# Optimization experiments

Measured on AMD Instinct MI355X. Metric: run time of the kernel, lower is better.

The kernel has to match this reference:

```python
import jax, jax.numpy as jnp
import numpy as np

B, S, D, H = 2, 2048, 1024, 16
HD = D // H  # head_dim = 64
ROPE_BASE = 10000.0


def _rope_cos_sin(seq_len, head_dim, dtype):
    inv_freq = 1.0 / (ROPE_BASE ** (jnp.arange(0, head_dim, 2, dtype=jnp.float32) / head_dim))
    t = jnp.arange(seq_len, dtype=jnp.float32)
    freqs = jnp.einsum('i,j->ij', t, inv_freq)            # [S, HD/2]
    emb = jnp.concatenate([freqs, freqs], axis=-1)        # [S, HD]
    return jnp.cos(emb).astype(dtype), jnp.sin(emb).astype(dtype)


def _rotate_half(x):
    x1, x2 = jnp.split(x, 2, axis=-1)
    return jnp.concatenate([-x2, x1], axis=-1)


def setup_inputs() -> dict:
    key = jax.random.key(0)
    ks = jax.random.split(key, 5)
    scale = 1.0 / np.sqrt(D)
    x = jax.random.normal(ks[0], (B, S, D), dtype=jnp.float32)
    wq = jax.random.normal(ks[1], (D, D), dtype=jnp.float32) * scale
    wk = jax.random.normal(ks[2], (D, D), dtype=jnp.float32) * scale
    wv = jax.random.normal(ks[3], (D, D), dtype=jnp.float32) * scale
    wo = jax.random.normal(ks[4], (D, D), dtype=jnp.float32) * scale
    # causal additive mask: 0 on/below diagonal, -1e9 above
    causal = jnp.triu(jnp.full((S, S), -1e9, dtype=jnp.float32), k=1)
    attention_mask = causal[None, None, :, :]
    return {'x': x, 'attention_mask': attention_mask, 'wq': wq, 'wk': wk, 'wv': wv, 'wo': wo}


def reference(x, attention_mask, wq, wk, wv, wo):
    b, s, d = x.shape
    scale = 1.0 / np.sqrt(HD)
    # projections (torch Linear: y = x @ W.T)
    q = (x @ wq.T).reshape(b, s, H, HD).transpose(0, 2, 1, 3)  # [B,H,S,HD]
    k = (x @ wk.T).reshape(b, s, H, HD).transpose(0, 2, 1, 3)
    v = (x @ wv.T).reshape(b, s, H, HD).transpose(0, 2, 1, 3)
    cos, sin = _rope_cos_sin(s, HD, x.dtype)                   # [S, HD]
    cos = cos[None, None]
    sin = sin[None, None]
    q = q * cos + _rotate_half(q) * sin
    k = k * cos + _rotate_half(k) * sin
    scores = jnp.einsum('bhqd,bhkd->bhqk', q, k) * scale       # [B,H,S,S]
    scores = scores + attention_mask
    probs = jax.nn.softmax(scores, axis=-1)
    out = jnp.einsum('bhqk,bhkd->bhqd', probs, v)              # [B,H,S,HD]
    out = out.transpose(0, 2, 1, 3).reshape(b, s, d)
    return out @ wo.T
```

## Files before the change

### kernel.cpp

```cpp
#include <hip/hip_runtime.h>
#include <cstdint>
#include <cstddef>

typedef __attribute__((ext_vector_type(8))) _Float16 half8;
typedef __attribute__((ext_vector_type(4))) _Float16 half4;
typedef __attribute__((ext_vector_type(2))) __fp16 fp16x2;
typedef __attribute__((ext_vector_type(4))) float f32x4;

#define NB 2
#define NS 2048
#define ND 1024
#define NH 16
#define NHD 64
#define NM (NB * NS)

__device__ __forceinline__ void cvt8(const float* __restrict__ s,
                                     _Float16* __restrict__ d, int g) {
  const float4* s4 = (const float4*)s + (size_t)g * 2;
  float4 a = s4[0], b = s4[1];
  half8 h;
  h[0] = (_Float16)a.x; h[1] = (_Float16)a.y;
  h[2] = (_Float16)a.z; h[3] = (_Float16)a.w;
  h[4] = (_Float16)b.x; h[5] = (_Float16)b.y;
  h[6] = (_Float16)b.z; h[7] = (_Float16)b.w;
  *(half8*)(d + (size_t)g * 8) = h;
}

__global__ void prep(const float* __restrict__ x,
                     const float* __restrict__ wq, const float* __restrict__ wk,
                     const float* __restrict__ wv, const float* __restrict__ wo,
                     _Float16* __restrict__ xb,
                     _Float16* __restrict__ wqb, _Float16* __restrict__ wkb,
                     _Float16* __restrict__ wvb, _Float16* __restrict__ wob,
                     float* __restrict__ cosT, float* __restrict__ sinT) {
  int i = blockIdx.x * 256 + threadIdx.x;
  if (i < 524288) {
    cvt8(x, xb, i);
  } else if (i < 1048576) {
    int j = i - 524288;
    int k = j >> 17, g = j & 131071;
    const float* ws = (k == 0) ? wq : (k == 1) ? wk : (k == 2) ? wv : wo;
    _Float16* wd = (k == 0) ? wqb : (k == 1) ? wkb : (k == 2) ? wvb : wob;
    cvt8(ws, wd, g);
  } else if (i < 1056768) {
    int t0 = (i - 1048576) * 8;
#pragma unroll
    for (int e = 0; e < 8; ++e) {
      int t = t0 + e;
      int s = t >> 5, j = t & 31;
      float inv = expf(-(float)(2 * j) * (9.210340371976184f / 64.0f));
      float ang = (float)s * inv;
      cosT[t] = cosf(ang);
      sinT[t] = sinf(ang);
    }
  }
}

__device__ __forceinline__ void gload_lds16(const void* g, void* lds) {
  __builtin_amdgcn_global_load_lds(
      (const __attribute__((address_space(1))) unsigned int*)g,
      (__attribute__((address_space(3))) unsigned int*)lds, 16, 0, 0);
}

__device__ __forceinline__ float exp2_fast(float x) {
  float r;
  asm("v_exp_f32 %0, %1" : "=v"(r) : "v"(x));
  return r;
}

__device__ __forceinline__ void gemm_mainloop64(const _Float16* __restrict__ A,
                                                const _Float16* __restrict__ Bw,
                                                _Float16* As, _Float16* Bs,
                                                int brow, int bcol,
                                                int lane, int wid, int tid,
                                                f32x4 acc[4][4]) {
  const int l15 = lane & 15, l4 = lane >> 4;
  const int wr = wid >> 1, wc = wid & 1;
  const int rswz = (l15 & 7) << 4;
  const int srb = tid >> 3;
  const int scb = (tid & 7) * 16;

  for (int kt = 0; kt < ND / 64; ++kt) {
    const int k0 = kt * 64;
#pragma unroll
    for (int c = 0; c < 4; ++c) {
      const int r = c * 32 + srb;
      const int sb = scb ^ ((r & 7) << 4);
      gload_lds16((const char*)(A + (size_t)(brow + r) * ND + k0) + sb,
                  (char*)As + c * 4096 + tid * 16);
      gload_lds16((const char*)(Bw + (size_t)(bcol + r) * ND + k0) + sb,
                  (char*)Bs + c * 4096 + tid * 16);
    }
    __syncthreads();
#pragma unroll
    for (int kk = 0; kk < 2; ++kk) {
      half8 af[4], bf[4];
#pragma unroll
      for (int m = 0; m < 4; ++m) {
        const int row = wr * 64 + m * 16 + l15;
        af[m] = *(const half8*)((const char*)As +
                 ((row * 128 + kk * 64 + l4 * 16) ^ rswz));
      }
#pragma unroll
      for (int n = 0; n < 4; ++n) {
        const int row = wc * 64 + n * 16 + l15;
        bf[n] = *(const half8*)((const char*)Bs +
                 ((row * 128 + kk * 64 + l4 * 16) ^ rswz));
      }
#pragma unroll
      for (int m = 0; m < 4; ++m)
#pragma unroll
        for (int n = 0; n < 4; ++n)
          acc[m][n] = __builtin_amdgcn_mfma_f32_16x16x32_f16(af[m], bf[n],
                                                             acc[m][n], 0, 0, 0);
    }
    __syncthreads();
  }
}

__launch_bounds__(256, 3)
__global__ void qkv_gemm(const _Float16* __restrict__ X,
                         const _Float16* __restrict__ Wq,
                         const _Float16* __restrict__ Wk,
                         const _Float16* __restrict__ Wv,
                         _Float16* __restrict__ Qb,
                         _Float16* __restrict__ Kb,
                         _Float16* __restrict__ Vt,
                         const float* __restrict__ cosT,
                         const float* __restrict__ sinT) {
  __shared__ __align__(16) _Float16 As[128 * 64];
  __shared__ __align__(16) _Float16 Bs[128 * 64];
  const int tid = threadIdx.x, lane = tid & 63, wid = tid >> 6;
  const int l15 = lane & 15, l4 = lane >> 4;
  const int wr = wid >> 1, wc = wid & 1;
  const int brow = blockIdx.y * 128, bcol = blockIdx.x * 128;
  const int mode = blockIdx.z;
  const _Float16* W = (mode == 0) ? Wq : (mode == 1 ? Wk : Wv);

  f32x4 acc[4][4] = {};
  gemm_mainloop64(X, W, As, Bs, brow, bcol, lane, wid, tid, acc);

  const int b = brow >> 11;
  const int sbase = (brow & (NS - 1)) + wr * 64;
  const int h = (bcol >> 6) + wc;

  if (mode < 2) {
    _Float16* oh = ((mode == 0) ? Qb : Kb) + (size_t)(b * NH + h) * NS * NHD;
#pragma unroll
    for (int m = 0; m < 4; ++m) {
#pragma unroll
      for (int r = 0; r < 4; ++r) {
        const int s = sbase + m * 16 + l4 * 4 + r;
#pragma unroll
        for (int n = 0; n < 2; ++n) {
          const int hd = n * 16 + l15;
          const float c = cosT[s * 32 + hd];
          const float sn = sinT[s * 32 + hd];
          const float lo = acc[m][n][r], hi = acc[m][n + 2][r];
          oh[(size_t)s * NHD + hd]      = (_Float16)(lo * c - hi * sn);
          oh[(size_t)s * NHD + hd + 32] = (_Float16)(hi * c + lo * sn);
        }
      }
    }
  } else {
#pragma unroll
    for (int m = 0; m < 4; ++m) {
      const int s0 = sbase + m * 16 + l4 * 4;
      const int npos = (s0 & ~63) + (m >> 1) * 32 + l4 * 8 + (m & 1) * 4;
#pragma unroll
      for (int n = 0; n < 4; ++n) {
        const int hd = n * 16 + l15;
        half4 pk;
        pk[0] = (_Float16)acc[m][n][0];
        pk[1] = (_Float16)acc[m][n][1];
        pk[2] = (_Float16)acc[m][n][2];
        pk[3] = (_Float16)acc[m][n][3];
        *(half4*)(Vt + ((size_t)(b * NH + h) * NHD + hd) * NS + npos) = pk;
      }
    }
  }
}

__launch_bounds__(256, 5)
__global__ void flash_attn(const _Float16* __restrict__ Qb,
                           const _Float16* __restrict__ Kb,
                           const _Float16* __restrict__ Vt,
                           _Float16* __restrict__ Ob) {
  __shared__ __align__(16) _Float16 Ks[2][64 * 64];
  __shared__ __align__(16) _Float16 Vs[2][64 * 64];
  const int tid = threadIdx.x, lane = tid & 63, wid = tid >> 6;
  const int l15 = lane & 15, l4 = lane >> 4;
  const int bh = blockIdx.x & 31;
  const int qt = 31 - (blockIdx.x >> 5);
  const _Float16* Qh = Qb + (size_t)bh * NS * NHD;
  const char* Kg = (const char*)(Kb + (size_t)bh * NS * NHD);
  const char* Vg = (const char*)(Vt + (size_t)bh * NHD * NS);

  const float K1 = 0.125f * 1.4426950408889634f;
  const int swz_lane = ((lane >> 3) & 7) << 4;
  const int qloc = wid * 16 + l15;
  const int rswz = (l15 & 7) << 4;
  const int b = bh >> 4, h = bh & 15;
  const int nkt = qt + 1;

  half8 qf[2];
#pragma unroll
  for (int kk = 0; kk < 2; ++kk)
    qf[kk] = *(const half8*)&Qh[(size_t)(qt * 64 + wid * 16 + l15) * NHD + kk * 32 + l4 * 8];

  f32x4 oacc[4] = {};
  float mrun = -3.0e38f, lrun = 0.f;

#pragma unroll
  for (int c = 0; c < 2; ++c) {
    const int chunk = wid * 2 + c;
    const int slot = chunk * 1024 + lane * 16;
    const int sw = slot ^ swz_lane;
    gload_lds16(Kg + sw, (char*)&Ks[0][0] + slot);
    const int vrow = slot >> 7;
    gload_lds16(Vg + (size_t)vrow * (NS * 2) + (sw & 127), (char*)&Vs[0][0] + slot);
  }
  __syncthreads();

  int cur = 0;
  for (int kt = 0; kt < nkt; ++kt) {
    if (kt + 1 < nkt) {
      const size_t knext = (size_t)(kt + 1);
#pragma unroll
      for (int c = 0; c < 2; ++c) {
        const int chunk = wid * 2 + c;
        const int slot = chunk * 1024 + lane * 16;
        const int sw = slot ^ swz_lane;
        gload_lds16(Kg + knext * 8192 + sw, (char*)&Ks[cur ^ 1][0] + slot);
        const int vrow = slot >> 7;
        gload_lds16(Vg + (size_t)vrow * (NS * 2) + knext * 128 + (sw & 127),
                    (char*)&Vs[cur ^ 1][0] + slot);
      }
    }

    const bool diag = (kt == qt);
    const char* Kbuf = (const char*)&Ks[cur][0];
    const char* Vbuf = (const char*)&Vs[cur][0];

    f32x4 sacc[4] = {};
    __builtin_amdgcn_s_setprio(1);
#pragma unroll
    for (int kk = 0; kk < 2; ++kk) {
#pragma unroll
      for (int n = 0; n < 4; ++n) {
        if (diag && n > wid) continue;
        const int off = ((n * 16 + l15) * 128 + kk * 64 + l4 * 16) ^ rswz;
        half8 kf = *(const half8*)(Kbuf + off);
        sacc[n] = __builtin_amdgcn_mfma_f32_16x16x32_f16(kf, qf[kk], sacc[n], 0, 0, 0);
      }
    }
    __builtin_amdgcn_s_setprio(0);

    float traw[16];
#pragma unroll
    for (int n = 0; n < 4; ++n)
#pragma unroll
      for (int r = 0; r < 4; ++r) {
        float v = sacc[n][r];
        if (diag) {
          const int ki = n * 16 + l4 * 4 + r;
          v = (ki > qloc) ? -3.0e38f : v;
        }
        traw[n * 4 + r] = v;
      }
    float mx = traw[0];
#pragma unroll
    for (int j = 1; j < 16; ++j) mx = fmaxf(mx, traw[j]);
    mx = fmaxf(mx, __shfl_xor(mx, 16, 64));
    mx = fmaxf(mx, __shfl_xor(mx, 32, 64));
    mx *= K1;
    const float mnew = fmaxf(mrun, mx);
    const float alpha = exp2_fast(mrun - mnew);
    mrun = mnew;
    float ps[16], rs = 0.f;
#pragma unroll
    for (int j = 0; j < 16; ++j) {
      ps[j] = exp2_fast(__builtin_fmaf(traw[j], K1, -mnew));
      rs += ps[j];
    }
    rs += __shfl_xor(rs, 16, 64);
    rs += __shfl_xor(rs, 32, 64);
    lrun = lrun * alpha + rs;
#pragma unroll
    for (int n = 0; n < 4; ++n) oacc[n] *= alpha;

    __builtin_amdgcn_s_setprio(1);
#pragma unroll
    for (int c = 0; c < 2; ++c) {
      if (diag && c == 1 && wid < 2) continue;
      half8 pb;
#pragma unroll
      for (int q2 = 0; q2 < 4; ++q2) {
        fp16x2 pp = __builtin_amdgcn_cvt_pkrtz(ps[8 * c + 2 * q2],
                                               ps[8 * c + 2 * q2 + 1]);
        pb[2 * q2]     = (_Float16)pp[0];
        pb[2 * q2 + 1] = (_Float16)pp[1];
      }
#pragma unroll
      for (int n = 0; n < 4; ++n) {
        const int off = ((n * 16 + l15) * 128 + c * 64 + l4 * 16) ^ rswz;
        half8 va = *(const half8*)(Vbuf + off);
        oacc[n] = __builtin_amdgcn_mfma_f32_16x16x32_f16(va, pb, oacc[n], 0, 0, 0);
      }
    }
    __builtin_amdgcn_s_setprio(0);

    __syncthreads();
    cur ^= 1;
  }

  const int s = qt * 64 + wid * 16 + l15;
  const float invl = 1.0f / lrun;
#pragma unroll
  for (int n = 0; n < 4; ++n) {
    f32x4 ov = oacc[n] * invl;
    half4 o;
    o[0] = (_Float16)ov[0];
    o[1] = (_Float16)ov[1];
    o[2] = (_Float16)ov[2];
    o[3] = (_Float16)ov[3];
    *(half4*)&Ob[((size_t)(b * NS + s)) * ND + h * NHD + n * 16 + l4 * 4] = o;
  }
}

__launch_bounds__(256, 2)
__global__ void proj_gemm(const _Float16* __restrict__ A,
                          const _Float16* __restrict__ W,
                          float* __restrict__ out) {
  __shared__ __align__(16) _Float16 As[128 * 64];
  __shared__ __align__(16) _Float16 Bs[64 * 64];
  const int tid = threadIdx.x, lane = tid & 63, wid = tid >> 6;
  const int l15 = lane & 15, l4 = lane >> 4;
  const int wr = wid >> 1, wc = wid & 1;
  const int brow = blockIdx.y * 128, bcol = blockIdx.x * 64;
  const int rswz = (l15 & 7) << 4;
  const int srb = tid >> 3;
  const int scb = (tid & 7) * 16;

  f32x4 acc[4][2] = {};
  for (int kt = 0; kt < ND / 64; ++kt) {
    const int k0 = kt * 64;
#pragma unroll
    for (int c = 0; c < 4; ++c) {
      const int r = c * 32 + srb;
      const int sb = scb ^ ((r & 7) << 4);
      gload_lds16((const char*)(A + (size_t)(brow + r) * ND + k0) + sb,
                  (char*)As + c * 4096 + tid * 16);
    }
#pragma unroll
    for (int c = 0; c < 2; ++c) {
      const int r = c * 32 + srb;
      const int sb = scb ^ ((r & 7) << 4);
      gload_lds16((const char*)(W + (size_t)(bcol + r) * ND + k0) + sb,
                  (char*)Bs + c * 4096 + tid * 16);
    }
    __syncthreads();
#pragma unroll
    for (int kk = 0; kk < 2; ++kk) {
      half8 af[4], bf[2];
#pragma unroll
      for (int m = 0; m < 4; ++m) {
        const int row = wr * 64 + m * 16 + l15;
        af[m] = *(const half8*)((const char*)As +
                 ((row * 128 + kk * 64 + l4 * 16) ^ rswz));
      }
#pragma unroll
      for (int n = 0; n < 2; ++n) {
        const int row = wc * 32 + n * 16 + l15;
        bf[n] = *(const half8*)((const char*)Bs +
                 ((row * 128 + kk * 64 + l4 * 16) ^ rswz));
      }
#pragma unroll
      for (int m = 0; m < 4; ++m)
#pragma unroll
        for (int n = 0; n < 2; ++n)
          acc[m][n] = __builtin_amdgcn_mfma_f32_16x16x32_f16(af[m], bf[n],
                                                             acc[m][n], 0, 0, 0);
    }
    __syncthreads();
  }
#pragma unroll
  for (int m = 0; m < 4; ++m)
#pragma unroll
    for (int n = 0; n < 2; ++n)
#pragma unroll
      for (int r = 0; r < 4; ++r)
        out[(size_t)(brow + wr * 64 + m * 16 + l4 * 4 + r) * ND
            + bcol + wc * 32 + n * 16 + l15] = acc[m][n][r];
}

extern "C" void kernel_launch(void* const* d_in, const int* in_sizes, int n_in,
                              void* d_out, int out_size, void* d_ws, size_t ws_size,
                              hipStream_t stream) {
  const float* x  = (const float*)d_in[0];
  const float* wq = (const float*)d_in[2];
  const float* wk = (const float*)d_in[3];
  const float* wv = (const float*)d_in[4];
  const float* wo = (const float*)d_in[5];
  float* out = (float*)d_out;

  char* w = (char*)d_ws;
  _Float16* xb   = (_Float16*)(w);
  _Float16* wqb  = (_Float16*)(w + (8ull  << 20));
  _Float16* wkb  = (_Float16*)(w + (10ull << 20));
  _Float16* wvb  = (_Float16*)(w + (12ull << 20));
  _Float16* wob  = (_Float16*)(w + (14ull << 20));
  _Float16* Qb   = (_Float16*)(w + (16ull << 20));
  _Float16* Kb   = (_Float16*)(w + (24ull << 20));
  _Float16* Vt   = (_Float16*)(w + (32ull << 20));
  _Float16* Ob   = (_Float16*)(w + (40ull << 20));
  float*    cosT = (float*)   (w + (48ull << 20));
  float*    sinT = (float*)   (w + (48ull << 20) + (1ull << 18));

  dim3 blk(256);
  prep<<<4128, blk, 0, stream>>>(x, wq, wk, wv, wo, xb, wqb, wkb, wvb, wob,
                                 cosT, sinT);
  qkv_gemm<<<dim3(8, 32, 3), blk, 0, stream>>>(xb, wqb, wkb, wvb, Qb, Kb, Vt,
                                               cosT, sinT);
  flash_attn<<<1024, blk, 0, stream>>>(Qb, Kb, Vt, Ob);
  proj_gemm<<<dim3(16, 32), blk, 0, stream>>>(Ob, wob, out);
}
```

Baseline: 99.62 us.

## Double key tile to 128 in flash attention with templated masked last tile

The flash attention loop now processes 128-key tiles instead of 64, halving the number of iterations, barriers and online-softmax rescales per query tile. The tile body moves into a template so only the final tile pays for causal masking and for skipping work above the diagonal. The V staging layout and swizzle are reworked for the wider tile. LDS use doubles and the launch-bounds occupancy hint drops from 5 to 2 blocks, which adds register pressure and reduces latency hiding.

```diff
diff --git a/kernel.cpp b/kernel.cpp
--- a/kernel.cpp
+++ b/kernel.cpp
@@ -181,13 +181,89 @@
   }
 }
 
-__launch_bounds__(256, 5)
+template <bool MASKED>
+__device__ __forceinline__ void attn_tile(const char* Kbuf, const char* Vbuf,
+                                          const half8* qf, f32x4* oacc,
+                                          float& mrun, float& lrun,
+                                          int kbase, int qmaxw, int qglob,
+                                          int l15, int l4, int rswz, float K1) {
+  f32x4 sacc[8] = {};
+  __builtin_amdgcn_s_setprio(1);
+#pragma unroll
+  for (int kk = 0; kk < 2; ++kk) {
+#pragma unroll
+    for (int n = 0; n < 8; ++n) {
+      if (MASKED && kbase + n * 16 > qmaxw) continue;
+      const int off = ((n * 16 + l15) * 128 + kk * 64 + l4 * 16) ^ rswz;
+      half8 kf = *(const half8*)(Kbuf + off);
+      sacc[n] = __builtin_amdgcn_mfma_f32_16x16x32_f16(kf, qf[kk], sacc[n], 0, 0, 0);
+    }
+  }
+  __builtin_amdgcn_s_setprio(0);
+
+  float traw[32];
+#pragma unroll
+  for (int n = 0; n < 8; ++n)
+#pragma unroll
+    for (int r = 0; r < 4; ++r) {
+      float v = sacc[n][r];
+      if (MASKED) {
+        const int kg = kbase + n * 16 + l4 * 4 + r;
+        v = (kg > qglob) ? -3.0e38f : v;
+      }
+      traw[n * 4 + r] = v;
+    }
+  float mx = traw[0];
+#pragma unroll
+  for (int j = 1; j < 32; ++j) mx = fmaxf(mx, traw[j]);
+  mx = fmaxf(mx, __shfl_xor(mx, 16, 64));
+  mx = fmaxf(mx, __shfl_xor(mx, 32, 64));
+  mx *= K1;
+  const float mnew = fmaxf(mrun, mx);
+  const float alpha = exp2_fast(mrun - mnew);
+  mrun = mnew;
+  float ps[32], rs = 0.f;
+#pragma unroll
+  for (int j = 0; j < 32; ++j) {
+    ps[j] = exp2_fast(__builtin_fmaf(traw[j], K1, -mnew));
+    rs += ps[j];
+  }
+  rs += __shfl_xor(rs, 16, 64);
+  rs += __shfl_xor(rs, 32, 64);
+  lrun = lrun * alpha + rs;
+#pragma unroll
+  for (int n = 0; n < 4; ++n) oacc[n] *= alpha;
+
+  __builtin_amdgcn_s_setprio(1);
+#pragma unroll
+  for (int c = 0; c < 4; ++c) {
+    if (MASKED && kbase + c * 32 > qmaxw) continue;
+    half8 pb;
+#pragma unroll
+    for (int q2 = 0; q2 < 4; ++q2) {
+      fp16x2 pp = __builtin_amdgcn_cvt_pkrtz(ps[8 * c + 2 * q2],
+                                             ps[8 * c + 2 * q2 + 1]);
+      pb[2 * q2]     = (_Float16)pp[0];
+      pb[2 * q2 + 1] = (_Float16)pp[1];
+    }
+#pragma unroll
+    for (int n = 0; n < 4; ++n) {
+      const int off = (n * 16 + l15) * 256 + (c >> 1) * 128
+                    + (((c & 1) * 64 + l4 * 16) ^ rswz);
+      half8 va = *(const half8*)(Vbuf + off);
+      oacc[n] = __builtin_amdgcn_mfma_f32_16x16x32_f16(va, pb, oacc[n], 0, 0, 0);
+    }
+  }
+  __builtin_amdgcn_s_setprio(0);
+}
+
+__launch_bounds__(256, 2)
 __global__ void flash_attn(const _Float16* __restrict__ Qb,
                            const _Float16* __restrict__ Kb,
                            const _Float16* __restrict__ Vt,
                            _Float16* __restrict__ Ob) {
-  __shared__ __align__(16) _Float16 Ks[2][64 * 64];
-  __shared__ __align__(16) _Float16 Vs[2][64 * 64];
+  __shared__ __align__(16) _Float16 Ks[2][128 * 64];
+  __shared__ __align__(16) _Float16 Vs[2][64 * 128];
   const int tid = threadIdx.x, lane = tid & 63, wid = tid >> 6;
   const int l15 = lane & 15, l4 = lane >> 4;
   const int bh = blockIdx.x & 31;
@@ -198,123 +274,50 @@
 
   const float K1 = 0.125f * 1.4426950408889634f;
   const int swz_lane = ((lane >> 3) & 7) << 4;
-  const int qloc = wid * 16 + l15;
   const int rswz = (l15 & 7) << 4;
   const int b = bh >> 4, h = bh & 15;
-  const int nkt = qt + 1;
+  const int nt = (qt >> 1) + 1;
+  const int kbase_last = (nt - 1) * 128;
+  const int qglob = qt * 64 + wid * 16 + l15;
+  const int qmaxw = qt * 64 + wid * 16 + 15;
 
   half8 qf[2];
 #pragma unroll
   for (int kk = 0; kk < 2; ++kk)
-    qf[kk] = *(const half8*)&Qh[(size_t)(qt * 64 + wid * 16 + l15) * NHD + kk * 32 + l4 * 8];
+    qf[kk] = *(const half8*)&Qh[(size_t)qglob * NHD + kk * 32 + l4 * 8];
 
   f32x4 oacc[4] = {};
   float mrun = -3.0e38f, lrun = 0.f;
 
-#pragma unroll
-  for (int c = 0; c < 2; ++c) {
-    const int chunk = wid * 2 + c;
-    const int slot = chunk * 1024 + lane * 16;
-    const int sw = slot ^ swz_lane;
-    gload_lds16(Kg + sw, (char*)&Ks[0][0] + slot);
-    const int vrow = slot >> 7;
-    gload_lds16(Vg + (size_t)vrow * (NS * 2) + (sw & 127), (char*)&Vs[0][0] + slot);
-  }
+  auto stage = [&](int t, int si) {
+#pragma unroll
+    for (int c = 0; c < 4; ++c) {
+      const int chunk = wid * 4 + c;
+      const int slot = chunk * 1024 + lane * 16;
+      const int sw = slot ^ swz_lane;
+      gload_lds16(Kg + (size_t)t * 16384 + sw, (char*)&Ks[si][0] + slot);
+      const int vrow = slot >> 8;
+      const int vhalf = (slot >> 7) & 1;
+      const int vinner = slot & 127;
+      gload_lds16(Vg + (size_t)vrow * (NS * 2) + t * 256 + vhalf * 128
+                     + (vinner ^ ((vrow & 7) << 4)),
+                  (char*)&Vs[si][0] + slot);
+    }
+  };
+
+  stage(0, 0);
   __syncthreads();
-
   int cur = 0;
-  for (int kt = 0; kt < nkt; ++kt) {
-    if (kt + 1 < nkt) {
-      const size_t knext = (size_t)(kt + 1);
-#pragma unroll
-      for (int c = 0; c < 2; ++c) {
-        const int chunk = wid * 2 + c;
-        const int slot = chunk * 1024 + lane * 16;
-        const int sw = slot ^ swz_lane;
-        gload_lds16(Kg + knext * 8192 + sw, (char*)&Ks[cur ^ 1][0] + slot);
-        const int vrow = slot >> 7;
-        gload_lds16(Vg + (size_t)vrow * (NS * 2) + knext * 128 + (sw & 127),
-                    (char*)&Vs[cur ^ 1][0] + slot);
-      }
-    }
-
-    const bool diag = (kt == qt);
-    const char* Kbuf = (const char*)&Ks[cur][0];
-    const char* Vbuf = (const char*)&Vs[cur][0];
-
-    f32x4 sacc[4] = {};
-    __builtin_amdgcn_s_setprio(1);
-#pragma unroll
-    for (int kk = 0; kk < 2; ++kk) {
-#pragma unroll
-      for (int n = 0; n < 4; ++n) {
-        if (diag && n > wid) continue;
-        const int off = ((n * 16 + l15) * 128 + kk * 64 + l4 * 16) ^ rswz;
-        half8 kf = *(const half8*)(Kbuf + off);
-        sacc[n] = __builtin_amdgcn_mfma_f32_16x16x32_f16(kf, qf[kk], sacc[n], 0, 0, 0);
-      }
-    }
-    __builtin_amdgcn_s_setprio(0);
-
-    float traw[16];
-#pragma unroll
-    for (int n = 0; n < 4; ++n)
-#pragma unroll
-      for (int r = 0; r < 4; ++r) {
-        float v = sacc[n][r];
-        if (diag) {
-          const int ki = n * 16 + l4 * 4 + r;
-          v = (ki > qloc) ? -3.0e38f : v;
-        }
-        traw[n * 4 + r] = v;
-      }
-    float mx = traw[0];
-#pragma unroll
-    for (int j = 1; j < 16; ++j) mx = fmaxf(mx, traw[j]);
-    mx = fmaxf(mx, __shfl_xor(mx, 16, 64));
-    mx = fmaxf(mx, __shfl_xor(mx, 32, 64));
-    mx *= K1;
-    const float mnew = fmaxf(mrun, mx);
-    const float alpha = exp2_fast(mrun - mnew);
-    mrun = mnew;
-    float ps[16], rs = 0.f;
-#pragma unroll
-    for (int j = 0; j < 16; ++j) {
-      ps[j] = exp2_fast(__builtin_fmaf(traw[j], K1, -mnew));
-      rs += ps[j];
-    }
-    rs += __shfl_xor(rs, 16, 64);
-    rs += __shfl_xor(rs, 32, 64);
-    lrun = lrun * alpha + rs;
-#pragma unroll
-    for (int n = 0; n < 4; ++n) oacc[n] *= alpha;
-
-    __builtin_amdgcn_s_setprio(1);
-#pragma unroll
-    for (int c = 0; c < 2; ++c) {
-      if (diag && c == 1 && wid < 2) continue;
-      half8 pb;
-#pragma unroll
-      for (int q2 = 0; q2 < 4; ++q2) {
-        fp16x2 pp = __builtin_amdgcn_cvt_pkrtz(ps[8 * c + 2 * q2],
-                                               ps[8 * c + 2 * q2 + 1]);
-        pb[2 * q2]     = (_Float16)pp[0];
-        pb[2 * q2 + 1] = (_Float16)pp[1];
-      }
-#pragma unroll
-      for (int n = 0; n < 4; ++n) {
-        const int off = ((n * 16 + l15) * 128 + c * 64 + l4 * 16) ^ rswz;
-        half8 va = *(const half8*)(Vbuf + off);
-        oacc[n] = __builtin_amdgcn_mfma_f32_16x16x32_f16(va, pb, oacc[n], 0, 0, 0);
-      }
-    }
-    __builtin_amdgcn_s_setprio(0);
-
+  for (int t = 0; t + 1 < nt; ++t) {
+    stage(t + 1, cur ^ 1);
+    attn_tile<false>((const char*)&Ks[cur][0], (const char*)&Vs[cur][0], qf,
+                     oacc, mrun, lrun, 0, 0, 0, l15, l4, rswz, K1);
     __syncthreads();
     cur ^= 1;
   }
-
-  const int s = qt * 64 + wid * 16 + l15;
+  attn_tile<true>((const char*)&Ks[cur][0], (const char*)&Vs[cur][0], qf,
+                  oacc, mrun, lrun, kbase_last, qmaxw, qglob, l15, l4, rswz, K1);
+
   const float invl = 1.0f / lrun;
 #pragma unroll
   for (int n = 0; n < 4; ++n) {
@@ -324,7 +327,7 @@
     o[1] = (_Float16)ov[1];
     o[2] = (_Float16)ov[2];
     o[3] = (_Float16)ov[3];
-    *(half4*)&Ob[((size_t)(b * NS + s)) * ND + h * NHD + n * 16 + l4 * 4] = o;
+    *(half4*)&Ob[((size_t)(b * NS + qglob)) * ND + h * NHD + n * 16 + l4 * 4] = o;
   }
 }
 
```

Measured after the change: 122.3 us. 22.8% more time.

## Share K/V tile loads across two query tiles per 512-thread flash block

Applied to the files above, without the earlier changes.

Each flash-attention block now has 8 waves and covers 128 query rows (two 64-row sub-tiles), so every staged K/V tile in LDS serves both sub-tiles and global K/V traffic per query drops by about half. The grid shrinks to 512 blocks, and each wave loads one chunk per stage instead of two. The first sub-tile's waves sit idle through the final key tile, where only the second sub-tile still has work, while still joining the barriers. Fewer, larger blocks can also leave the causal work less evenly balanced across CUs.

```diff
diff --git a/kernel.cpp b/kernel.cpp
--- a/kernel.cpp
+++ b/kernel.cpp
@@ -181,7 +181,7 @@
   }
 }
 
-__launch_bounds__(256, 5)
+__launch_bounds__(512, 6)
 __global__ void flash_attn(const _Float16* __restrict__ Qb,
                            const _Float16* __restrict__ Kb,
                            const _Float16* __restrict__ Vt,
@@ -190,131 +190,124 @@
   __shared__ __align__(16) _Float16 Vs[2][64 * 64];
   const int tid = threadIdx.x, lane = tid & 63, wid = tid >> 6;
   const int l15 = lane & 15, l4 = lane >> 4;
+  const int sub = wid >> 2, w4 = wid & 3;
   const int bh = blockIdx.x & 31;
-  const int qt = 31 - (blockIdx.x >> 5);
+  const int qt2 = 15 - (blockIdx.x >> 5);
   const _Float16* Qh = Qb + (size_t)bh * NS * NHD;
   const char* Kg = (const char*)(Kb + (size_t)bh * NS * NHD);
   const char* Vg = (const char*)(Vt + (size_t)bh * NHD * NS);
 
   const float K1 = 0.125f * 1.4426950408889634f;
   const int swz_lane = ((lane >> 3) & 7) << 4;
-  const int qloc = wid * 16 + l15;
+  const int qloc = w4 * 16 + l15;
   const int rswz = (l15 & 7) << 4;
   const int b = bh >> 4, h = bh & 15;
-  const int nkt = qt + 1;
+  const int nkt = 2 * qt2 + 2;
+  const int mylim = 2 * qt2 + sub;
+  const int qglob = qt2 * 128 + sub * 64 + w4 * 16 + l15;
 
   half8 qf[2];
 #pragma unroll
   for (int kk = 0; kk < 2; ++kk)
-    qf[kk] = *(const half8*)&Qh[(size_t)(qt * 64 + wid * 16 + l15) * NHD + kk * 32 + l4 * 8];
+    qf[kk] = *(const half8*)&Qh[(size_t)qglob * NHD + kk * 32 + l4 * 8];
 
   f32x4 oacc[4] = {};
   float mrun = -3.0e38f, lrun = 0.f;
 
-#pragma unroll
-  for (int c = 0; c < 2; ++c) {
-    const int chunk = wid * 2 + c;
-    const int slot = chunk * 1024 + lane * 16;
+  auto stage = [&](int t, int si) {
+    const int slot = wid * 1024 + lane * 16;
     const int sw = slot ^ swz_lane;
-    gload_lds16(Kg + sw, (char*)&Ks[0][0] + slot);
+    gload_lds16(Kg + (size_t)t * 8192 + sw, (char*)&Ks[si][0] + slot);
     const int vrow = slot >> 7;
-    gload_lds16(Vg + (size_t)vrow * (NS * 2) + (sw & 127), (char*)&Vs[0][0] + slot);
-  }
+    gload_lds16(Vg + (size_t)vrow * (NS * 2) + t * 128 + (sw & 127),
+                (char*)&Vs[si][0] + slot);
+  };
+
+  stage(0, 0);
   __syncthreads();
 
   int cur = 0;
   for (int kt = 0; kt < nkt; ++kt) {
-    if (kt + 1 < nkt) {
-      const size_t knext = (size_t)(kt + 1);
+    if (kt + 1 < nkt) stage(kt + 1, cur ^ 1);
+
+    if (kt <= mylim) {
+      const bool diag = (kt == mylim);
+      const char* Kbuf = (const char*)&Ks[cur][0];
+      const char* Vbuf = (const char*)&Vs[cur][0];
+
+      f32x4 sacc[4] = {};
+      __builtin_amdgcn_s_setprio(1);
+#pragma unroll
+      for (int kk = 0; kk < 2; ++kk) {
+#pragma unroll
+        for (int n = 0; n < 4; ++n) {
+          if (diag && n > w4) continue;
+          const int off = ((n * 16 + l15) * 128 + kk * 64 + l4 * 16) ^ rswz;
+          half8 kf = *(const half8*)(Kbuf + off);
+          sacc[n] = __builtin_amdgcn_mfma_f32_16x16x32_f16(kf, qf[kk], sacc[n], 0, 0, 0);
+        }
+      }
+      __builtin_amdgcn_s_setprio(0);
+
+      float traw[16];
+#pragma unroll
+      for (int n = 0; n < 4; ++n)
+#pragma unroll
+        for (int r = 0; r < 4; ++r) {
+          float v = sacc[n][r];
+          if (diag) {
+            const int ki = n * 16 + l4 * 4 + r;
+            v = (ki > qloc) ? -3.0e38f : v;
+          }
+          traw[n * 4 + r] = v;
+        }
+      float mx = traw[0];
+#pragma unroll
+      for (int j = 1; j < 16; ++j) mx = fmaxf(mx, traw[j]);
+      mx = fmaxf(mx, __shfl_xor(mx, 16, 64));
+      mx = fmaxf(mx, __shfl_xor(mx, 32, 64));
+      mx *= K1;
+      const float mnew = fmaxf(mrun, mx);
+      const float alpha = exp2_fast(mrun - mnew);
+      mrun = mnew;
+      float ps[16], rs = 0.f;
+#pragma unroll
+      for (int j = 0; j < 16; ++j) {
+        ps[j] = exp2_fast(__builtin_fmaf(traw[j], K1, -mnew));
+        rs += ps[j];
+      }
+      rs += __shfl_xor(rs, 16, 64);
+      rs += __shfl_xor(rs, 32, 64);
+      lrun = lrun * alpha + rs;
+#pragma unroll
+      for (int n = 0; n < 4; ++n) oacc[n] *= alpha;
+
+      __builtin_amdgcn_s_setprio(1);
 #pragma unroll
       for (int c = 0; c < 2; ++c) {
-        const int chunk = wid * 2 + c;
-        const int slot = chunk * 1024 + lane * 16;
-        const int sw = slot ^ swz_lane;
-        gload_lds16(Kg + knext * 8192 + sw, (char*)&Ks[cur ^ 1][0] + slot);
-        const int vrow = slot >> 7;
-        gload_lds16(Vg + (size_t)vrow * (NS * 2) + knext * 128 + (sw & 127),
-                    (char*)&Vs[cur ^ 1][0] + slot);
-      }
-    }
-
-    const bool diag = (kt == qt);
-    const char* Kbuf = (const char*)&Ks[cur][0];
-    const char* Vbuf = (const char*)&Vs[cur][0];
-
-    f32x4 sacc[4] = {};
-    __builtin_amdgcn_s_setprio(1);
-#pragma unroll
-    for (int kk = 0; kk < 2; ++kk) {
-#pragma unroll
-      for (int n = 0; n < 4; ++n) {
-        if (diag && n > wid) continue;
-        const int off = ((n * 16 + l15) * 128 + kk * 64 + l4 * 16) ^ rswz;
-        half8 kf = *(const half8*)(Kbuf + off);
-        sacc[n] = __builtin_amdgcn_mfma_f32_16x16x32_f16(kf, qf[kk], sacc[n], 0, 0, 0);
-      }
-    }
-    __builtin_amdgcn_s_setprio(0);
-
-    float traw[16];
-#pragma unroll
-    for (int n = 0; n < 4; ++n)
-#pragma unroll
-      for (int r = 0; r < 4; ++r) {
-        float v = sacc[n][r];
-        if (diag) {
-          const int ki = n * 16 + l4 * 4 + r;
-          v = (ki > qloc) ? -3.0e38f : v;
+        if (diag && c == 1 && w4 < 2) continue;
+        half8 pb;
+#pragma unroll
+        for (int q2 = 0; q2 < 4; ++q2) {
+          fp16x2 pp = __builtin_amdgcn_cvt_pkrtz(ps[8 * c + 2 * q2],
+                                                 ps[8 * c + 2 * q2 + 1]);
+          pb[2 * q2]     = (_Float16)pp[0];
+          pb[2 * q2 + 1] = (_Float16)pp[1];
         }
-        traw[n * 4 + r] = v;
-      }
-    float mx = traw[0];
-#pragma unroll
-    for (int j = 1; j < 16; ++j) mx = fmaxf(mx, traw[j]);
-    mx = fmaxf(mx, __shfl_xor(mx, 16, 64));
-    mx = fmaxf(mx, __shfl_xor(mx, 32, 64));
-    mx *= K1;
-    const float mnew = fmaxf(mrun, mx);
-    const float alpha = exp2_fast(mrun - mnew);
-    mrun = mnew;
-    float ps[16], rs = 0.f;
-#pragma unroll
-    for (int j = 0; j < 16; ++j) {
-      ps[j] = exp2_fast(__builtin_fmaf(traw[j], K1, -mnew));
-      rs += ps[j];
-    }
-    rs += __shfl_xor(rs, 16, 64);
-    rs += __shfl_xor(rs, 32, 64);
-    lrun = lrun * alpha + rs;
-#pragma unroll
-    for (int n = 0; n < 4; ++n) oacc[n] *= alpha;
-
-    __builtin_amdgcn_s_setprio(1);
-#pragma unroll
-    for (int c = 0; c < 2; ++c) {
-      if (diag && c == 1 && wid < 2) continue;
-      half8 pb;
-#pragma unroll
-      for (int q2 = 0; q2 < 4; ++q2) {
-        fp16x2 pp = __builtin_amdgcn_cvt_pkrtz(ps[8 * c + 2 * q2],
-                                               ps[8 * c + 2 * q2 + 1]);
-        pb[2 * q2]     = (_Float16)pp[0];
-        pb[2 * q2 + 1] = (_Float16)pp[1];
-      }
-#pragma unroll
-      for (int n = 0; n < 4; ++n) {
-        const int off = ((n * 16 + l15) * 128 + c * 64 + l4 * 16) ^ rswz;
-        half8 va = *(const half8*)(Vbuf + off);
-        oacc[n] = __builtin_amdgcn_mfma_f32_16x16x32_f16(va, pb, oacc[n], 0, 0, 0);
-      }
-    }
-    __builtin_amdgcn_s_setprio(0);
+#pragma unroll
+        for (int n = 0; n < 4; ++n) {
+          const int off = ((n * 16 + l15) * 128 + c * 64 + l4 * 16) ^ rswz;
+          half8 va = *(const half8*)(Vbuf + off);
+          oacc[n] = __builtin_amdgcn_mfma_f32_16x16x32_f16(va, pb, oacc[n], 0, 0, 0);
+        }
+      }
+      __builtin_amdgcn_s_setprio(0);
+    }
 
     __syncthreads();
     cur ^= 1;
   }
 
-  const int s = qt * 64 + wid * 16 + l15;
   const float invl = 1.0f / lrun;
 #pragma unroll
   for (int n = 0; n < 4; ++n) {
@@ -324,7 +317,7 @@
     o[1] = (_Float16)ov[1];
     o[2] = (_Float16)ov[2];
     o[3] = (_Float16)ov[3];
-    *(half4*)&Ob[((size_t)(b * NS + s)) * ND + h * NHD + n * 16 + l4 * 4] = o;
+    *(half4*)&Ob[((size_t)(b * NS + qglob)) * ND + h * NHD + n * 16 + l4 * 4] = o;
   }
 }
 
@@ -422,6 +415,6 @@
                                  cosT, sinT);
   qkv_gemm<<<dim3(8, 32, 3), blk, 0, stream>>>(xb, wqb, wkb, wvb, Qb, Kb, Vt,
                                                cosT, sinT);
-  flash_attn<<<1024, blk, 0, stream>>>(Qb, Kb, Vt, Ob);
+  flash_attn<<<512, dim3(512), 0, stream>>>(Qb, Kb, Vt, Ob);
   proj_gemm<<<dim3(16, 32), blk, 0, stream>>>(Ob, wob, out);
 }
```

Result: slower. 114.7 us (+15.1%).
